# Kernel optimization log

Hardware: AMD Instinct MI355X
Metric: run time of the kernel (lower is better)

Reference implementation:

```python
import jax, jax.numpy as jnp
import numpy as np

ALPHA = 0.5  # trapezoidal_alpha

def rmsnorm(x, w, eps=1e-5):
    return x * jax.lax.rsqrt(jnp.mean(x * x, axis=-1, keepdims=True) + eps) * w

def ssd_scan(x, Bc, Cc, dt, A, alpha):
    # x: (B,L,H,P), Bc/Cc: (B,L,N), dt: (B,L,H), A: (H,)
    da = jnp.exp(dt * A)  # (B,L,H), A < 0 so da in (0,1)
    shift = lambda t: jnp.concatenate([jnp.zeros_like(t[:, :1]), t[:, :-1]], axis=1)
    xp, bp, dtp = shift(x), shift(Bc), shift(dt)
    to_t = lambda t: jnp.moveaxis(t, 1, 0)
    xs = tuple(map(to_t, (x, Bc, Cc, dt, da, xp, bp, dtp)))
    Bb, _, H, P = x.shape
    N = Bc.shape[-1]
    h0 = jnp.zeros((Bb, H, P, N), x.dtype)
    def step(h, inp):
        xt, bt, ct, dtt, dat, xpt, bpt, dtpt = inp
        u = dtt[:, :, None, None] * xt[..., None] * bt[:, None, None, :]      # (B,H,P,N)
        up = dtpt[:, :, None, None] * xpt[..., None] * bpt[:, None, None, :]  # prev input term
        h = dat[:, :, None, None] * (h + alpha * up) + (1.0 - alpha) * u      # trapezoidal update
        y = jnp.einsum('bhpn,bn->bhp', h, ct)
        return h, y
    _, ys = jax.lax.scan(step, h0, xs)
    return jnp.moveaxis(ys, 0, 1)  # (B,L,H,P)

def setup_inputs() -> dict:
    key = jax.random.key(0)
    ks = jax.random.split(key, 10)
    B, NV, NQ = 4, 256, 32
    D, DI, H, N, E, NL = 1024, 2048, 32, 128, 1536, 12
    PROJ = 2 * DI + 2 * N + H  # z | x | B | C | dt
    s = 0.02
    return {
        'visual_tokens': jax.random.normal(ks[0], (B, NV, D), jnp.float32),
        'query_embeds': jax.random.normal(ks[1], (B, NQ, D), jnp.float32),
        'vis_w': jax.random.normal(ks[2], (D, D), jnp.float32) * s,
        'vis_b': jnp.zeros((D,), jnp.float32),
        'qry_w': jax.random.normal(ks[3], (D, D), jnp.float32) * s,
        'qry_b': jnp.zeros((D,), jnp.float32),
        'norm_ws': jnp.ones((NL, D), jnp.float32),
        'in_ws': jax.random.normal(ks[4], (NL, D, PROJ), jnp.float32) * s,
        'dt_biases': jax.random.normal(ks[5], (NL, H), jnp.float32) * 0.5,
        'A_logs': jnp.log(jnp.tile(jnp.arange(1.0, H + 1.0, dtype=jnp.float32)[None], (NL, 1))),
        'D_ssm': jnp.ones((NL, H), jnp.float32),
        'gnorm_ws': jnp.ones((NL, DI), jnp.float32),
        'out_ws': jax.random.normal(ks[6], (NL, DI, D), jnp.float32) * s,
        'norm_f_w': jnp.ones((D,), jnp.float32),
        'head_w': jax.random.normal(ks[7], (D, E), jnp.float32) * s,
        'head_b': jnp.zeros((E,), jnp.float32),
    }

def reference(visual_tokens, query_embeds, vis_w, vis_b, qry_w, qry_b, norm_ws, in_ws,
              dt_biases, A_logs, D_ssm, gnorm_ws, out_ws, norm_f_w, head_w, head_b):
    vis = visual_tokens @ vis_w + vis_b
    qry = query_embeds @ qry_w + qry_b
    hidden = jnp.concatenate([vis, qry], axis=1)  # (B,L,D)
    n_layers = in_ws.shape[0]
    d_inner = gnorm_ws.shape[-1]
    H = A_logs.shape[-1]
    P = d_inner // H
    N = (in_ws.shape[-1] - 2 * d_inner - H) // 2
    for i in range(n_layers):
        res = hidden
        xin = rmsnorm(hidden, norm_ws[i])
        proj = xin @ in_ws[i]  # (B,L,2*DI+2*N+H)
        z = proj[..., :d_inner]
        xss = proj[..., d_inner:2 * d_inner]
        Bc = proj[..., 2 * d_inner:2 * d_inner + N]
        Cc = proj[..., 2 * d_inner + N:2 * d_inner + 2 * N]
        dt = jax.nn.softplus(proj[..., 2 * d_inner + 2 * N:] + dt_biases[i])
        A = -jnp.exp(A_logs[i])
        xr = xss.reshape(xss.shape[0], xss.shape[1], H, P)
        y = ssd_scan(xr, Bc, Cc, dt, A, ALPHA) + D_ssm[i][None, None, :, None] * xr
        y = y.reshape(xss.shape)
        y = rmsnorm(y * jax.nn.silu(z), gnorm_ws[i])  # gated RMSNorm
        hidden = res + y @ out_ws[i]
    hidden = rmsnorm(hidden, norm_f_w)
    pooled = hidden.mean(axis=1)                   # (B,D)
    out = pooled @ head_w + head_b                 # (B,E)
    nrm = jnp.linalg.norm(out, axis=-1, keepdims=True)
    return out / jnp.maximum(nrm, 1e-12)           # F.normalize semantics
```

## Files before the change

kernel.cpp:

```cpp
#include <hip/hip_runtime.h>
#include <cmath>

#define Bb   4
#define Tt   288
#define Dd   1024
#define DIi  2048
#define HH   32
#define PP   64
#define NNs  128
#define PROJ  4384
#define PROJP 4480
#define NLl  12
#define EE   1536

typedef __bf16 bf16x8 __attribute__((ext_vector_type(8)));
typedef float f32x4 __attribute__((ext_vector_type(4)));

__device__ __forceinline__ unsigned short f2bf(float v) {
  __bf16 b = (__bf16)v;
  return __builtin_bit_cast(unsigned short, b);
}
__device__ __forceinline__ float bf2f(unsigned short u) {
  unsigned int x = ((unsigned int)u) << 16;
  return __builtin_bit_cast(float, x);
}
__device__ __forceinline__ void split2(float v, unsigned short& h, unsigned short& l) {
  h = f2bf(v);
  l = f2bf(v - bf2f(h));
}

__device__ __forceinline__ void async16(const void* g, void* l) {
  __builtin_amdgcn_global_load_lds(
      (const __attribute__((address_space(1))) unsigned int*)g,
      (__attribute__((address_space(3))) unsigned int*)l, 16, 0, 0);
}

__device__ inline float block_reduce_sum(float v, float* lds) {
#pragma unroll
  for (int d = 32; d > 0; d >>= 1) v += __shfl_down(v, d, 64);
  int lane = threadIdx.x & 63;
  int w = threadIdx.x >> 6;
  if (lane == 0) lds[w] = v;
  __syncthreads();
  if (threadIdx.x == 0) {
    float s = lds[0];
    int nw = blockDim.x >> 6;
    for (int i = 1; i < nw; i++) s += lds[i];
    lds[0] = s;
  }
  __syncthreads();
  return lds[0];
}

__global__ __launch_bounds__(256) void cvt_act2_k(const float* __restrict__ x,
                                                  unsigned short* __restrict__ oh,
                                                  unsigned short* __restrict__ ol, int n) {
  int idx = (blockIdx.x * 256 + threadIdx.x) * 4;
  if (idx >= n) return;
  float4 v = *(const float4*)&x[idx];
  ushort4 h, l;
  split2(v.x, h.x, l.x); split2(v.y, h.y, l.y);
  split2(v.z, h.z, l.z); split2(v.w, h.w, l.w);
  *(ushort4*)&oh[idx] = h;
  *(ushort4*)&ol[idx] = l;
}

__global__ __launch_bounds__(256) void cvt_tr2_k(const float* __restrict__ W,
                                                 unsigned short* __restrict__ Wth,
                                                 unsigned short* __restrict__ Wtl,
                                                 int K, int N) {
  __shared__ float tile[32][33];
  const int n0 = blockIdx.x * 32, k0 = blockIdx.y * 32;
  const int c = threadIdx.x & 31;
  const int r0 = threadIdx.x >> 5;
#pragma unroll
  for (int j = 0; j < 4; j++) {
    int r = r0 + j * 8;
    int n = n0 + c;
    tile[r][c] = (n < N) ? W[(size_t)(k0 + r) * N + n] : 0.f;
  }
  __syncthreads();
  const int nl = threadIdx.x >> 3;
  const int kl = (threadIdx.x & 7) * 4;
  ushort4 h, l;
  split2(tile[kl + 0][nl], h.x, l.x);
  split2(tile[kl + 1][nl], h.y, l.y);
  split2(tile[kl + 2][nl], h.z, l.z);
  split2(tile[kl + 3][nl], h.w, l.w);
  size_t o = (size_t)(n0 + nl) * K + k0 + kl;
  *(ushort4*)&Wth[o] = h;
  *(ushort4*)&Wtl[o] = l;
}

template<int BM, int BN>
__global__ __launch_bounds__(256) void gemm3_k(
    const unsigned short* __restrict__ Ah, const unsigned short* __restrict__ Al,
    const unsigned short* __restrict__ Wh, const unsigned short* __restrict__ Wl,
    const float* __restrict__ bias, const float* __restrict__ res,
    float* __restrict__ C, int M, int N, int K,
    int rows_per_b, int T_total, int t_off)
{
  constexpr int FM = BM / 32;
  constexpr int FN = BN / 32;
  __shared__ __align__(16) unsigned short Ash[BM * 32];
  __shared__ __align__(16) unsigned short Asl[BM * 32];
  __shared__ __align__(16) unsigned short Bsh[BN * 32];
  __shared__ __align__(16) unsigned short Bsl[BN * 32];
  const int tid = threadIdx.x;
  const int lane = tid & 63;
  const int wm = (tid >> 6) >> 1;
  const int wn = (tid >> 6) & 1;
  const int m0 = blockIdx.y * BM;
  const int n0 = blockIdx.x * BN;
  const int lrow = lane & 15;
  const int lkb = (lane >> 4) * 8;

  f32x4 acc[FM][FN];
#pragma unroll
  for (int i = 0; i < FM; i++)
#pragma unroll
    for (int j = 0; j < FN; j++) acc[i][j] = (f32x4)0.0f;

  for (int k0 = 0; k0 < K; k0 += 32) {
#pragma unroll
    for (int c = 0; c < BM / 64; c++) {
      int o = (c * 256 + tid) * 16;
      int row = o >> 6;
      int colb = o & 63;
      size_t gb = ((size_t)(m0 + row) * K + k0) * 2 + colb;
      async16((const char*)Ah + gb, (char*)Ash + o);
      async16((const char*)Al + gb, (char*)Asl + o);
    }
#pragma unroll
    for (int c = 0; c < BN / 64; c++) {
      int o = (c * 256 + tid) * 16;
      int row = o >> 6;
      int colb = o & 63;
      size_t gb = ((size_t)(n0 + row) * K + k0) * 2 + colb;
      async16((const char*)Wh + gb, (char*)Bsh + o);
      async16((const char*)Wl + gb, (char*)Bsl + o);
    }
    __syncthreads();

    bf16x8 ah[FM], al[FM], bh[FN], bl[FN];
#pragma unroll
    for (int i = 0; i < FM; i++) {
      int off = (wm * (FM * 16) + i * 16 + lrow) * 32 + lkb;
      ah[i] = *(const bf16x8*)&Ash[off];
      al[i] = *(const bf16x8*)&Asl[off];
    }
#pragma unroll
    for (int j = 0; j < FN; j++) {
      int off = (wn * (FN * 16) + j * 16 + lrow) * 32 + lkb;
      bh[j] = *(const bf16x8*)&Bsh[off];
      bl[j] = *(const bf16x8*)&Bsl[off];
    }
#pragma unroll
    for (int i = 0; i < FM; i++)
#pragma unroll
      for (int j = 0; j < FN; j++) {
        acc[i][j] = __builtin_amdgcn_mfma_f32_16x16x32_bf16(ah[i], bh[j], acc[i][j], 0, 0, 0);
        acc[i][j] = __builtin_amdgcn_mfma_f32_16x16x32_bf16(ah[i], bl[j], acc[i][j], 0, 0, 0);
        acc[i][j] = __builtin_amdgcn_mfma_f32_16x16x32_bf16(al[i], bh[j], acc[i][j], 0, 0, 0);
      }
    __syncthreads();
  }

  const int erow = (lane >> 4) * 4;
#pragma unroll
  for (int i = 0; i < FM; i++) {
    int mbase = m0 + wm * (FM * 16) + i * 16 + erow;
#pragma unroll
    for (int j = 0; j < FN; j++) {
      int ncol = n0 + wn * (FN * 16) + j * 16 + lrow;
      float bv = bias ? bias[ncol] : 0.f;
#pragma unroll
      for (int e = 0; e < 4; e++) {
        int m = mbase + e;
        size_t orow;
        if (T_total) {
          int bbv = m / rows_per_b;
          orow = (size_t)bbv * T_total + (m - bbv * rows_per_b) + t_off;
        } else {
          orow = (size_t)m;
        }
        float v = acc[i][j][e] + bv;
        if (res) v += res[orow * N + ncol];
        C[orow * N + ncol] = v;
      }
    }
  }
}

__global__ __launch_bounds__(256) void gemm_k(
    const float* __restrict__ A, const float* __restrict__ W,
    const float* __restrict__ bias, const float* __restrict__ res,
    float* __restrict__ C, int M, int N, int K,
    int rows_per_b, int T_total, int t_off)
{
  __shared__ float As[16][64];
  __shared__ float Ws[16][64];
  const int tid = threadIdx.x;
  const int tx = tid & 15;
  const int ty = tid >> 4;
  const int m0 = blockIdx.y * 64;
  const int n0 = blockIdx.x * 64;
  float acc[4][4] = {};
  const int ar = tid >> 2;
  const int ac = (tid & 3) << 2;
  const int wr = tid >> 4;
  const int wc = (tid & 15) << 2;

  for (int k0 = 0; k0 < K; k0 += 16) {
    float4 av = {0.f, 0.f, 0.f, 0.f};
    int gr = m0 + ar;
    if (gr < M) av = *(const float4*)&A[(size_t)gr * K + k0 + ac];
    As[ac + 0][ar] = av.x; As[ac + 1][ar] = av.y;
    As[ac + 2][ar] = av.z; As[ac + 3][ar] = av.w;

    float4 wv = {0.f, 0.f, 0.f, 0.f};
    int gc = n0 + wc;
    const float* wp = &W[(size_t)(k0 + wr) * N + gc];
    if (gc + 3 < N) {
      wv = *(const float4*)wp;
    } else {
      if (gc + 0 < N) wv.x = wp[0];
      if (gc + 1 < N) wv.y = wp[1];
      if (gc + 2 < N) wv.z = wp[2];
    }
    *(float4*)&Ws[wr][wc] = wv;
    __syncthreads();
#pragma unroll
    for (int kk = 0; kk < 16; kk++) {
      float4 a4 = *(const float4*)&As[kk][ty << 2];
      float4 b4 = *(const float4*)&Ws[kk][tx << 2];
      float a[4] = {a4.x, a4.y, a4.z, a4.w};
      float b[4] = {b4.x, b4.y, b4.z, b4.w};
#pragma unroll
      for (int i = 0; i < 4; i++)
#pragma unroll
        for (int j = 0; j < 4; j++)
          acc[i][j] = fmaf(a[i], b[j], acc[i][j]);
    }
    __syncthreads();
  }
#pragma unroll
  for (int i = 0; i < 4; i++) {
    int gr = m0 + (ty << 2) + i;
    if (gr >= M) continue;
    int bbv = gr / rows_per_b;
    int tt = gr - bbv * rows_per_b;
    size_t orow = (size_t)bbv * T_total + tt + t_off;
#pragma unroll
    for (int j = 0; j < 4; j++) {
      int gc = n0 + (tx << 2) + j;
      if (gc >= N) continue;
      float v = acc[i][j];
      if (bias) v += bias[gc];
      if (res)  v += res[orow * (size_t)N + gc];
      C[orow * (size_t)N + gc] = v;
    }
  }
}

__global__ __launch_bounds__(256) void rmsnorm_k(
    const float* __restrict__ x, const float* __restrict__ w, float* __restrict__ out)
{
  __shared__ float lds[8];
  const int row = blockIdx.x;
  const float* xr = x + (size_t)row * Dd;
  float4 v = *(const float4*)&xr[threadIdx.x << 2];
  float ss = v.x * v.x + v.y * v.y + v.z * v.z + v.w * v.w;
  ss = block_reduce_sum(ss, lds);
  float sc = rsqrtf(ss * (1.f / Dd) + 1e-5f);
  float4 wv = *(const float4*)&w[threadIdx.x << 2];
  float4 o = {v.x * sc * wv.x, v.y * sc * wv.y, v.z * sc * wv.z, v.w * sc * wv.w};
  *(float4*)&out[(size_t)row * Dd + (threadIdx.x << 2)] = o;
}

__global__ __launch_bounds__(256) void rmsnorm2_k(
    const float* __restrict__ x, const float* __restrict__ w,
    unsigned short* __restrict__ oh, unsigned short* __restrict__ ol)
{
  __shared__ float lds[8];
  const int row = blockIdx.x;
  const float* xr = x + (size_t)row * Dd;
  float4 v = *(const float4*)&xr[threadIdx.x << 2];
  float ss = v.x * v.x + v.y * v.y + v.z * v.z + v.w * v.w;
  ss = block_reduce_sum(ss, lds);
  float sc = rsqrtf(ss * (1.f / Dd) + 1e-5f);
  float4 wv = *(const float4*)&w[threadIdx.x << 2];
  ushort4 h, l;
  split2(v.x * sc * wv.x, h.x, l.x);
  split2(v.y * sc * wv.y, h.y, l.y);
  split2(v.z * sc * wv.z, h.z, l.z);
  split2(v.w * sc * wv.w, h.w, l.w);
  size_t o = (size_t)row * Dd + (threadIdx.x << 2);
  *(ushort4*)&oh[o] = h;
  *(ushort4*)&ol[o] = l;
}

__global__ __launch_bounds__(64) void dtcum_k(
    const float* __restrict__ proj, const float* __restrict__ dt_bias,
    const float* __restrict__ A_log,
    float* __restrict__ dtt, double* __restrict__ dcum)
{
  const int h = blockIdx.x & 31;
  const int b = blockIdx.x >> 5;
  const int lane = threadIdx.x;
  const float A = -expf(A_log[h]);
  const float bias = dt_bias[h];
  const int rowo = (b * HH + h) * Tt;
  double base = 0.0;
  for (int c = 0; c < (Tt + 63) / 64; c++) {
    int t = c * 64 + lane;
    float dt = 0.f;
    if (t < Tt) {
      float v = proj[(size_t)(b * Tt + t) * PROJP + 2 * DIi + 2 * NNs + h] + bias;
      dt = (v > 20.f) ? v : log1pf(expf(v));
    }
    double a = (double)(dt * A);
#pragma unroll
    for (int d = 1; d < 64; d <<= 1) {
      double o = __shfl_up(a, d, 64);
      if (lane >= d) a += o;
    }
    double cum = base + a;
    if (t < Tt) { dtt[rowo + t] = dt; dcum[rowo + t] = cum; }
    base = __shfl(cum, 63, 64);
  }
}

__global__ __launch_bounds__(256) void cbgemm_k(const float* __restrict__ proj,
                                                float* __restrict__ St)
{
  const int tI = blockIdx.x, jI = blockIdx.y, b = blockIdx.z;
  if (jI > tI) return;
  __shared__ float Ct[32][130];
  __shared__ float Bt[32][130];
  const int tid = threadIdx.x;
  const int r = tid >> 3;
  const int q = (tid & 7) * 16;
  const float* pb = proj + (size_t)b * Tt * PROJP;
  {
    const float* crow = pb + (size_t)(tI * 32 + r) * PROJP + 2 * DIi + NNs + q;
    const float* brow = pb + (size_t)(jI * 32 + r) * PROJP + 2 * DIi + q;
#pragma unroll
    for (int f = 0; f < 16; f += 4) {
      float4 c4 = *(const float4*)&crow[f];
      float4 b4 = *(const float4*)&brow[f];
      *(float2*)&Ct[r][q + f]     = make_float2(c4.x, c4.y);
      *(float2*)&Ct[r][q + f + 2] = make_float2(c4.z, c4.w);
      *(float2*)&Bt[r][q + f]     = make_float2(b4.x, b4.y);
      *(float2*)&Bt[r][q + f + 2] = make_float2(b4.z, b4.w);
    }
  }
  __syncthreads();
  const int j_r = tid >> 3;
  const int t_c = (tid & 7) * 4;
  float acc[4] = {0.f, 0.f, 0.f, 0.f};
  for (int n = 0; n < NNs; n += 2) {
    float2 b2 = *(const float2*)&Bt[j_r][n];
#pragma unroll
    for (int k = 0; k < 4; k++) {
      float2 c2 = *(const float2*)&Ct[t_c + k][n];
      acc[k] = fmaf(b2.x, c2.x, acc[k]);
      acc[k] = fmaf(b2.y, c2.y, acc[k]);
    }
  }
  float* so = St + ((size_t)b * Tt + jI * 32 + j_r) * Tt + tI * 32 + t_c;
  *(float4*)so = make_float4(acc[0], acc[1], acc[2], acc[3]);
}

__global__ __launch_bounds__(256) void ssd_y_k(
    const float* __restrict__ proj, const float* __restrict__ St,
    const float* __restrict__ dtt, const double* __restrict__ dcum,
    const float* __restrict__ Dssm, float* __restrict__ ybuf)
{
  const int tI = blockIdx.x;
  const int h  = blockIdx.y;
  const int b  = blockIdx.z;
  __shared__ __align__(16) float Xs[32][64];
  __shared__ __align__(16) float Ss[32][36];
  __shared__ double cjs[32];
  const int tid = threadIdx.x;
  const int t_l = tid & 31;
  const int pg  = tid >> 5;
  const int t0  = tI * 32;
  const int rowo = (b * HH + h) * Tt;
  const double ct = dcum[rowo + t0 + t_l];
  const float Ds = Dssm[h];
  const float* pb = proj + (size_t)b * Tt * PROJP;
  float y[8] = {0,0,0,0,0,0,0,0};
  const int sr = tid >> 3;
  const int sq = tid & 7;

  for (int jI = 0; jI <= tI; jI++) {
    const int j0 = jI * 32;
    {
      const float* xr = pb + (size_t)(j0 + sr) * PROJP + DIi + h * PP + sq * 8;
      *(float4*)&Xs[sr][sq * 8]     = *(const float4*)&xr[0];
      *(float4*)&Xs[sr][sq * 8 + 4] = *(const float4*)&xr[4];
    }
    {
      const float* srow = St + ((size_t)b * Tt + j0 + sr) * Tt + t0 + sq * 4;
      float4 s4 = *(const float4*)srow;
      float dj = dtt[rowo + j0 + sr];
      s4.x *= dj; s4.y *= dj; s4.z *= dj; s4.w *= dj;
      *(float4*)&Ss[sr][sq * 4] = s4;
    }
    if (tid < 32) cjs[tid] = dcum[rowo + j0 + tid];
    __syncthreads();

    if (jI < tI) {
#pragma unroll 4
      for (int j = 0; j < 32; j++) {
        float d = (float)(ct - cjs[j]);
        float m = Ss[j][t_l] * expf(fminf(d, 0.f));
        const float* xp = &Xs[j][pg * 8];
        float4 a0 = *(const float4*)&xp[0];
        float4 a1 = *(const float4*)&xp[4];
        y[0] = fmaf(m, a0.x, y[0]); y[1] = fmaf(m, a0.y, y[1]);
        y[2] = fmaf(m, a0.z, y[2]); y[3] = fmaf(m, a0.w, y[3]);
        y[4] = fmaf(m, a1.x, y[4]); y[5] = fmaf(m, a1.y, y[5]);
        y[6] = fmaf(m, a1.z, y[6]); y[7] = fmaf(m, a1.w, y[7]);
      }
    } else {
      for (int j = 0; j < 32; j++) {
        float sv = Ss[j][t_l];
        float d = (float)(ct - cjs[j]);
        float m = sv * expf(fminf(d, 0.f));
        if (j == t_l) m = 0.5f * sv + Ds;
        if (j > t_l)  m = 0.f;
        const float* xp = &Xs[j][pg * 8];
        float4 a0 = *(const float4*)&xp[0];
        float4 a1 = *(const float4*)&xp[4];
        y[0] = fmaf(m, a0.x, y[0]); y[1] = fmaf(m, a0.y, y[1]);
        y[2] = fmaf(m, a0.z, y[2]); y[3] = fmaf(m, a0.w, y[3]);
        y[4] = fmaf(m, a1.x, y[4]); y[5] = fmaf(m, a1.y, y[5]);
        y[6] = fmaf(m, a1.z, y[6]); y[7] = fmaf(m, a1.w, y[7]);
      }
    }
    __syncthreads();
  }
  float* yo = &ybuf[(size_t)(b * Tt + t0 + t_l) * DIi + h * PP + pg * 8];
  *(float4*)&yo[0] = make_float4(y[0], y[1], y[2], y[3]);
  *(float4*)&yo[4] = make_float4(y[4], y[5], y[6], y[7]);
}

__global__ __launch_bounds__(256) void gate_norm2_k(
    const float* __restrict__ ybuf, const float* __restrict__ proj,
    const float* __restrict__ gw,
    unsigned short* __restrict__ yh, unsigned short* __restrict__ yl)
{
  __shared__ float lds[8];
  const int row = blockIdx.x;
  const float* yr = ybuf + (size_t)row * DIi;
  const float* zr = proj + (size_t)row * PROJP;
  const int base = threadIdx.x << 3;
  float4 z0 = *(const float4*)&zr[base];
  float4 z1 = *(const float4*)&zr[base + 4];
  float4 y0 = *(const float4*)&yr[base];
  float4 y1 = *(const float4*)&yr[base + 4];
  float zz[8] = {z0.x, z0.y, z0.z, z0.w, z1.x, z1.y, z1.z, z1.w};
  float yy[8] = {y0.x, y0.y, y0.z, y0.w, y1.x, y1.y, y1.z, y1.w};
  float g[8];
  float ss = 0.f;
#pragma unroll
  for (int e = 0; e < 8; e++) {
    float s = zz[e] / (1.f + expf(-zz[e]));
    float gv = yy[e] * s;
    g[e] = gv;
    ss += gv * gv;
  }
  ss = block_reduce_sum(ss, lds);
  float sc = rsqrtf(ss * (1.f / DIi) + 1e-5f);
  ushort4 h0, l0, h1, l1;
  split2(g[0] * sc * gw[base + 0], h0.x, l0.x);
  split2(g[1] * sc * gw[base + 1], h0.y, l0.y);
  split2(g[2] * sc * gw[base + 2], h0.z, l0.z);
  split2(g[3] * sc * gw[base + 3], h0.w, l0.w);
  split2(g[4] * sc * gw[base + 4], h1.x, l1.x);
  split2(g[5] * sc * gw[base + 5], h1.y, l1.y);
  split2(g[6] * sc * gw[base + 6], h1.z, l1.z);
  split2(g[7] * sc * gw[base + 7], h1.w, l1.w);
  size_t o = (size_t)row * DIi + base;
  *(ushort4*)&yh[o] = h0; *(ushort4*)&yh[o + 4] = h1;
  *(ushort4*)&yl[o] = l0; *(ushort4*)&yl[o + 4] = l1;
}

__global__ void pool_k(const float* __restrict__ xin, float* __restrict__ pooled) {
  int b = blockIdx.x;
  int d = blockIdx.y * 256 + threadIdx.x;
  const float* base = xin + (size_t)b * Tt * Dd + d;
  float s = 0.f;
  for (int t = 0; t < Tt; t++) s += base[(size_t)t * Dd];
  pooled[b * Dd + d] = s * (1.f / Tt);
}

__global__ __launch_bounds__(256) void l2norm_k(float* __restrict__ out) {
  __shared__ float lds[8];
  const int row = blockIdx.x;
  float* r = out + (size_t)row * EE;
  float v[6];
  float ss = 0.f;
#pragma unroll
  for (int e = 0; e < 6; e++) {
    v[e] = r[(e << 8) + threadIdx.x];
    ss += v[e] * v[e];
  }
  ss = block_reduce_sum(ss, lds);
  float sc = 1.f / fmaxf(sqrtf(ss), 1e-12f);
#pragma unroll
  for (int e = 0; e < 6; e++) r[(e << 8) + threadIdx.x] = v[e] * sc;
}

extern "C" void kernel_launch(void* const* d_in, const int* in_sizes, int n_in,
                              void* d_out, int out_size, void* d_ws, size_t ws_size,
                              hipStream_t stream) {
  (void)in_sizes; (void)n_in; (void)out_size; (void)ws_size;
  const float* visual   = (const float*)d_in[0];
  const float* query    = (const float*)d_in[1];
  const float* vis_w    = (const float*)d_in[2];
  const float* vis_b    = (const float*)d_in[3];
  const float* qry_w    = (const float*)d_in[4];
  const float* qry_b    = (const float*)d_in[5];
  const float* norm_ws  = (const float*)d_in[6];
  const float* in_ws    = (const float*)d_in[7];
  const float* dt_biases= (const float*)d_in[8];
  const float* A_logs   = (const float*)d_in[9];
  const float* D_ssm    = (const float*)d_in[10];
  const float* gnorm_ws = (const float*)d_in[11];
  const float* out_ws   = (const float*)d_in[12];
  const float* norm_f_w = (const float*)d_in[13];
  const float* head_w   = (const float*)d_in[14];
  const float* head_b   = (const float*)d_in[15];
  float* out = (float*)d_out;

  char* w = (char*)d_ws;
  float*          hidden = (float*)w;          w += (size_t)1152 * 1024 * 4;
  unsigned short* xh     = (unsigned short*)w; w += (size_t)1152 * 1024 * 2;
  unsigned short* xl     = (unsigned short*)w; w += (size_t)1152 * 1024 * 2;
  float*          proj   = (float*)w;          w += (size_t)1152 * PROJP * 4;
  float*          ybuf   = (float*)w;          w += (size_t)1152 * 2048 * 4;
  unsigned short* yh     = (unsigned short*)w; w += (size_t)1152 * 2048 * 2;
  unsigned short* yl     = (unsigned short*)w; w += (size_t)1152 * 2048 * 2;
  float*          dtt    = (float*)w;          w += (size_t)Bb * HH * Tt * 4;
  double*         dcum   = (double*)w;         w += (size_t)Bb * HH * Tt * 8;
  float*          Stb    = (float*)w;          w += (size_t)Bb * Tt * Tt * 4;
  float*          pooled = (float*)w;          w += (size_t)4096 * 4;
  unsigned short* wth    = (unsigned short*)w; w += (size_t)PROJP * 1024 * 2;
  unsigned short* wtl    = (unsigned short*)w; w += (size_t)PROJP * 1024 * 2;

  dim3 blk(256);

  cvt_act2_k<<<1024, blk, 0, stream>>>(visual, xh, xl, 1024 * 1024);
  cvt_act2_k<<<128, blk, 0, stream>>>(query, xh + (size_t)1024 * 1024,
                                      xl + (size_t)1024 * 1024, 128 * 1024);
  cvt_tr2_k<<<dim3(32, 32), blk, 0, stream>>>(vis_w, wth, wtl, 1024, 1024);
  gemm3_k<64, 64><<<dim3(16, 16), blk, 0, stream>>>(
      xh, xl, wth, wtl, vis_b, nullptr, hidden, 1024, 1024, 1024, 256, Tt, 0);
  cvt_tr2_k<<<dim3(32, 32), blk, 0, stream>>>(qry_w, wth, wtl, 1024, 1024);
  gemm3_k<64, 64><<<dim3(16, 2), blk, 0, stream>>>(
      xh + (size_t)1024 * 1024, xl + (size_t)1024 * 1024, wth, wtl,
      qry_b, nullptr, hidden, 128, 1024, 1024, 32, Tt, 256);

  for (int i = 0; i < NLl; i++) {
    rmsnorm2_k<<<Bb * Tt, blk, 0, stream>>>(hidden, norm_ws + i * Dd, xh, xl);
    cvt_tr2_k<<<dim3(PROJP / 32, 32), blk, 0, stream>>>(
        in_ws + (size_t)i * Dd * PROJ, wth, wtl, Dd, PROJ);
    gemm3_k<128, 128><<<dim3(PROJP / 128, 9), blk, 0, stream>>>(
        xh, xl, wth, wtl, nullptr, nullptr, proj, 1152, PROJP, Dd, 1152, 0, 0);
    dtcum_k<<<Bb * HH, dim3(64), 0, stream>>>(proj, dt_biases + i * HH,
                                              A_logs + i * HH, dtt, dcum);
    cbgemm_k<<<dim3(9, 9, Bb), blk, 0, stream>>>(proj, Stb);
    ssd_y_k<<<dim3(9, HH, Bb), blk, 0, stream>>>(proj, Stb, dtt, dcum,
                                                 D_ssm + i * HH, ybuf);
    gate_norm2_k<<<Bb * Tt, blk, 0, stream>>>(ybuf, proj, gnorm_ws + i * DIi, yh, yl);
    cvt_tr2_k<<<dim3(32, 64), blk, 0, stream>>>(
        out_ws + (size_t)i * DIi * Dd, wth, wtl, DIi, Dd);
    gemm3_k<64, 64><<<dim3(16, 18), blk, 0, stream>>>(
        yh, yl, wth, wtl, nullptr, hidden, hidden, 1152, Dd, DIi, 1152, 0, 0);
  }

  rmsnorm_k<<<Bb * Tt, blk, 0, stream>>>(hidden, norm_f_w, ybuf);
  pool_k<<<dim3(Bb, 4), blk, 0, stream>>>(ybuf, pooled);
  gemm_k<<<dim3(24, 1), blk, 0, stream>>>(pooled, head_w, head_b, nullptr, out,
                                          Bb, EE, Dd, Bb, 0, 0);
  l2norm_k<<<Bb, blk, 0, stream>>>(out);
}
```

Measured before the change: 2.777 ms.

## Use 32x32 MFMA tiles, batch weight conversions upfront, merge activation conversion

Switches the split-bf16 GEMM from 16x16x32 to 32x32x16 MFMA fragments, which changes the per-wave fragment layout and the epilogue indexing. When the workspace is large enough, all layer weights are transposed and split in a few batched launches before the layer loop instead of one conversion per GEMM. The two activation conversion launches are also merged into one. Together these aim to cut launch count and raise MFMA efficiency, at the cost of a much larger workspace and a different accumulator register footprint.

```diff
diff --git a/kernel.cpp b/kernel.cpp
--- a/kernel.cpp
+++ b/kernel.cpp
@@ -15,6 +15,7 @@
 
 typedef __bf16 bf16x8 __attribute__((ext_vector_type(8)));
 typedef float f32x4 __attribute__((ext_vector_type(4)));
+typedef float f32x16 __attribute__((ext_vector_type(16)));
 
 __device__ __forceinline__ unsigned short f2bf(float v) {
   __bf16 b = (__bf16)v;
@@ -52,12 +53,13 @@
   return lds[0];
 }
 
-__global__ __launch_bounds__(256) void cvt_act2_k(const float* __restrict__ x,
-                                                  unsigned short* __restrict__ oh,
-                                                  unsigned short* __restrict__ ol, int n) {
+__global__ __launch_bounds__(256) void cvt_act_k(const float* __restrict__ vis,
+                                                 const float* __restrict__ qry,
+                                                 unsigned short* __restrict__ oh,
+                                                 unsigned short* __restrict__ ol) {
   int idx = (blockIdx.x * 256 + threadIdx.x) * 4;
-  if (idx >= n) return;
-  float4 v = *(const float4*)&x[idx];
+  const float* src = (idx < 1024 * 1024) ? &vis[idx] : &qry[idx - 1024 * 1024];
+  float4 v = *(const float4*)src;
   ushort4 h, l;
   split2(v.x, h.x, l.x); split2(v.y, h.y, l.y);
   split2(v.z, h.z, l.z); split2(v.w, h.w, l.w);
@@ -68,8 +70,12 @@
 __global__ __launch_bounds__(256) void cvt_tr2_k(const float* __restrict__ W,
                                                  unsigned short* __restrict__ Wth,
                                                  unsigned short* __restrict__ Wtl,
-                                                 int K, int N) {
+                                                 int K, int N,
+                                                 size_t wstride, size_t ostride) {
   __shared__ float tile[32][33];
+  W   += (size_t)blockIdx.z * wstride;
+  Wth += (size_t)blockIdx.z * ostride;
+  Wtl += (size_t)blockIdx.z * ostride;
   const int n0 = blockIdx.x * 32, k0 = blockIdx.y * 32;
   const int c = threadIdx.x & 31;
   const int r0 = threadIdx.x >> 5;
@@ -100,8 +106,8 @@
     float* __restrict__ C, int M, int N, int K,
     int rows_per_b, int T_total, int t_off)
 {
-  constexpr int FM = BM / 32;
-  constexpr int FN = BN / 32;
+  constexpr int FM = BM / 64;
+  constexpr int FN = BN / 64;
   __shared__ __align__(16) unsigned short Ash[BM * 32];
   __shared__ __align__(16) unsigned short Asl[BM * 32];
   __shared__ __align__(16) unsigned short Bsh[BN * 32];
@@ -112,14 +118,14 @@
   const int wn = (tid >> 6) & 1;
   const int m0 = blockIdx.y * BM;
   const int n0 = blockIdx.x * BN;
-  const int lrow = lane & 15;
-  const int lkb = (lane >> 4) * 8;
-
-  f32x4 acc[FM][FN];
+  const int lrow = lane & 31;
+  const int lkb = (lane >> 5) * 8;
+
+  f32x16 acc[FM][FN];
 #pragma unroll
   for (int i = 0; i < FM; i++)
 #pragma unroll
-    for (int j = 0; j < FN; j++) acc[i][j] = (f32x4)0.0f;
+    for (int j = 0; j < FN; j++) acc[i][j] = (f32x16)0.0f;
 
   for (int k0 = 0; k0 < K; k0 += 32) {
 #pragma unroll
@@ -142,41 +148,43 @@
     }
     __syncthreads();
 
-    bf16x8 ah[FM], al[FM], bh[FN], bl[FN];
-#pragma unroll
-    for (int i = 0; i < FM; i++) {
-      int off = (wm * (FM * 16) + i * 16 + lrow) * 32 + lkb;
-      ah[i] = *(const bf16x8*)&Ash[off];
-      al[i] = *(const bf16x8*)&Asl[off];
-    }
+#pragma unroll
+    for (int kh = 0; kh < 2; kh++) {
+      bf16x8 ah[FM], al[FM], bh[FN], bl[FN];
+#pragma unroll
+      for (int i = 0; i < FM; i++) {
+        int off = (wm * (BM / 2) + i * 32 + lrow) * 32 + kh * 16 + lkb;
+        ah[i] = *(const bf16x8*)&Ash[off];
+        al[i] = *(const bf16x8*)&Asl[off];
+      }
+#pragma unroll
+      for (int j = 0; j < FN; j++) {
+        int off = (wn * (BN / 2) + j * 32 + lrow) * 32 + kh * 16 + lkb;
+        bh[j] = *(const bf16x8*)&Bsh[off];
+        bl[j] = *(const bf16x8*)&Bsl[off];
+      }
+#pragma unroll
+      for (int i = 0; i < FM; i++)
+#pragma unroll
+        for (int j = 0; j < FN; j++) {
+          acc[i][j] = __builtin_amdgcn_mfma_f32_32x32x16_bf16(ah[i], bh[j], acc[i][j], 0, 0, 0);
+          acc[i][j] = __builtin_amdgcn_mfma_f32_32x32x16_bf16(ah[i], bl[j], acc[i][j], 0, 0, 0);
+          acc[i][j] = __builtin_amdgcn_mfma_f32_32x32x16_bf16(al[i], bh[j], acc[i][j], 0, 0, 0);
+        }
+    }
+    __syncthreads();
+  }
+
+  const int r0 = (lane >> 5) * 4;
+#pragma unroll
+  for (int i = 0; i < FM; i++) {
 #pragma unroll
     for (int j = 0; j < FN; j++) {
-      int off = (wn * (FN * 16) + j * 16 + lrow) * 32 + lkb;
-      bh[j] = *(const bf16x8*)&Bsh[off];
-      bl[j] = *(const bf16x8*)&Bsl[off];
-    }
-#pragma unroll
-    for (int i = 0; i < FM; i++)
-#pragma unroll
-      for (int j = 0; j < FN; j++) {
-        acc[i][j] = __builtin_amdgcn_mfma_f32_16x16x32_bf16(ah[i], bh[j], acc[i][j], 0, 0, 0);
-        acc[i][j] = __builtin_amdgcn_mfma_f32_16x16x32_bf16(ah[i], bl[j], acc[i][j], 0, 0, 0);
-        acc[i][j] = __builtin_amdgcn_mfma_f32_16x16x32_bf16(al[i], bh[j], acc[i][j], 0, 0, 0);
-      }
-    __syncthreads();
-  }
-
-  const int erow = (lane >> 4) * 4;
-#pragma unroll
-  for (int i = 0; i < FM; i++) {
-    int mbase = m0 + wm * (FM * 16) + i * 16 + erow;
-#pragma unroll
-    for (int j = 0; j < FN; j++) {
-      int ncol = n0 + wn * (FN * 16) + j * 16 + lrow;
+      int ncol = n0 + wn * (BN / 2) + j * 32 + lrow;
       float bv = bias ? bias[ncol] : 0.f;
 #pragma unroll
-      for (int e = 0; e < 4; e++) {
-        int m = mbase + e;
+      for (int rg = 0; rg < 16; rg++) {
+        int m = m0 + wm * (BM / 2) + i * 32 + (rg & 3) + 8 * (rg >> 2) + r0;
         size_t orow;
         if (T_total) {
           int bbv = m / rows_per_b;
@@ -184,7 +192,7 @@
         } else {
           orow = (size_t)m;
         }
-        float v = acc[i][j][e] + bv;
+        float v = acc[i][j][rg] + bv;
         if (res) v += res[orow * N + ncol];
         C[orow * N + ncol] = v;
       }
@@ -518,7 +526,7 @@
 extern "C" void kernel_launch(void* const* d_in, const int* in_sizes, int n_in,
                               void* d_out, int out_size, void* d_ws, size_t ws_size,
                               hipStream_t stream) {
-  (void)in_sizes; (void)n_in; (void)out_size; (void)ws_size;
+  (void)in_sizes; (void)n_in; (void)out_size;
   const float* visual   = (const float*)d_in[0];
   const float* query    = (const float*)d_in[1];
   const float* vis_w    = (const float*)d_in[2];
@@ -552,35 +560,72 @@
   unsigned short* wth    = (unsigned short*)w; w += (size_t)PROJP * 1024 * 2;
   unsigned short* wtl    = (unsigned short*)w; w += (size_t)PROJP * 1024 * 2;
 
+  unsigned short* wtin_h  = (unsigned short*)w; w += (size_t)NLl * PROJP * 1024 * 2;
+  unsigned short* wtin_l  = (unsigned short*)w; w += (size_t)NLl * PROJP * 1024 * 2;
+  unsigned short* wtout_h = (unsigned short*)w; w += (size_t)NLl * 1024 * 2048 * 2;
+  unsigned short* wtout_l = (unsigned short*)w; w += (size_t)NLl * 1024 * 2048 * 2;
+  unsigned short* wtv_h   = (unsigned short*)w; w += (size_t)1024 * 1024 * 2;
+  unsigned short* wtv_l   = (unsigned short*)w; w += (size_t)1024 * 1024 * 2;
+  unsigned short* wtq_h   = (unsigned short*)w; w += (size_t)1024 * 1024 * 2;
+  unsigned short* wtq_l   = (unsigned short*)w; w += (size_t)1024 * 1024 * 2;
+  const bool batched = ((size_t)(w - (char*)d_ws)) <= ws_size;
+
   dim3 blk(256);
 
-  cvt_act2_k<<<1024, blk, 0, stream>>>(visual, xh, xl, 1024 * 1024);
-  cvt_act2_k<<<128, blk, 0, stream>>>(query, xh + (size_t)1024 * 1024,
-                                      xl + (size_t)1024 * 1024, 128 * 1024);
-  cvt_tr2_k<<<dim3(32, 32), blk, 0, stream>>>(vis_w, wth, wtl, 1024, 1024);
-  gemm3_k<64, 64><<<dim3(16, 16), blk, 0, stream>>>(
-      xh, xl, wth, wtl, vis_b, nullptr, hidden, 1024, 1024, 1024, 256, Tt, 0);
-  cvt_tr2_k<<<dim3(32, 32), blk, 0, stream>>>(qry_w, wth, wtl, 1024, 1024);
-  gemm3_k<64, 64><<<dim3(16, 2), blk, 0, stream>>>(
-      xh + (size_t)1024 * 1024, xl + (size_t)1024 * 1024, wth, wtl,
-      qry_b, nullptr, hidden, 128, 1024, 1024, 32, Tt, 256);
+  cvt_act_k<<<1152, blk, 0, stream>>>(visual, query, xh, xl);
+
+  if (batched) {
+    cvt_tr2_k<<<dim3(32, 32, 1), blk, 0, stream>>>(vis_w, wtv_h, wtv_l, 1024, 1024, 0, 0);
+    cvt_tr2_k<<<dim3(32, 32, 1), blk, 0, stream>>>(qry_w, wtq_h, wtq_l, 1024, 1024, 0, 0);
+    cvt_tr2_k<<<dim3(PROJP / 32, 32, NLl), blk, 0, stream>>>(
+        in_ws, wtin_h, wtin_l, Dd, PROJ, (size_t)Dd * PROJ, (size_t)PROJP * 1024);
+    cvt_tr2_k<<<dim3(32, 64, NLl), blk, 0, stream>>>(
+        out_ws, wtout_h, wtout_l, DIi, Dd, (size_t)DIi * Dd, (size_t)1024 * 2048);
+    gemm3_k<64, 64><<<dim3(16, 16), blk, 0, stream>>>(
+        xh, xl, wtv_h, wtv_l, vis_b, nullptr, hidden, 1024, 1024, 1024, 256, Tt, 0);
+    gemm3_k<64, 64><<<dim3(16, 2), blk, 0, stream>>>(
+        xh + (size_t)1024 * 1024, xl + (size_t)1024 * 1024, wtq_h, wtq_l,
+        qry_b, nullptr, hidden, 128, 1024, 1024, 32, Tt, 256);
+  } else {
+    cvt_tr2_k<<<dim3(32, 32, 1), blk, 0, stream>>>(vis_w, wth, wtl, 1024, 1024, 0, 0);
+    gemm3_k<64, 64><<<dim3(16, 16), blk, 0, stream>>>(
+        xh, xl, wth, wtl, vis_b, nullptr, hidden, 1024, 1024, 1024, 256, Tt, 0);
+    cvt_tr2_k<<<dim3(32, 32, 1), blk, 0, stream>>>(qry_w, wth, wtl, 1024, 1024, 0, 0);
+    gemm3_k<64, 64><<<dim3(16, 2), blk, 0, stream>>>(
+        xh + (size_t)1024 * 1024, xl + (size_t)1024 * 1024, wth, wtl,
+        qry_b, nullptr, hidden, 128, 1024, 1024, 32, Tt, 256);
+  }
 
   for (int i = 0; i < NLl; i++) {
     rmsnorm2_k<<<Bb * Tt, blk, 0, stream>>>(hidden, norm_ws + i * Dd, xh, xl);
-    cvt_tr2_k<<<dim3(PROJP / 32, 32), blk, 0, stream>>>(
-        in_ws + (size_t)i * Dd * PROJ, wth, wtl, Dd, PROJ);
+    const unsigned short *bih, *bil;
+    if (batched) {
+      bih = wtin_h + (size_t)i * PROJP * 1024;
+      bil = wtin_l + (size_t)i * PROJP * 1024;
+    } else {
+      cvt_tr2_k<<<dim3(PROJP / 32, 32, 1), blk, 0, stream>>>(
+          in_ws + (size_t)i * Dd * PROJ, wth, wtl, Dd, PROJ, 0, 0);
+      bih = wth; bil = wtl;
+    }
     gemm3_k<128, 128><<<dim3(PROJP / 128, 9), blk, 0, stream>>>(
-        xh, xl, wth, wtl, nullptr, nullptr, proj, 1152, PROJP, Dd, 1152, 0, 0);
+        xh, xl, bih, bil, nullptr, nullptr, proj, 1152, PROJP, Dd, 1152, 0, 0);
     dtcum_k<<<Bb * HH, dim3(64), 0, stream>>>(proj, dt_biases + i * HH,
                                               A_logs + i * HH, dtt, dcum);
     cbgemm_k<<<dim3(9, 9, Bb), blk, 0, stream>>>(proj, Stb);
     ssd_y_k<<<dim3(9, HH, Bb), blk, 0, stream>>>(proj, Stb, dtt, dcum,
                                                  D_ssm + i * HH, ybuf);
     gate_norm2_k<<<Bb * Tt, blk, 0, stream>>>(ybuf, proj, gnorm_ws + i * DIi, yh, yl);
-    cvt_tr2_k<<<dim3(32, 64), blk, 0, stream>>>(
-        out_ws + (size_t)i * DIi * Dd, wth, wtl, DIi, Dd);
+    const unsigned short *boh, *bol;
+    if (batched) {
+      boh = wtout_h + (size_t)i * 1024 * 2048;
+      bol = wtout_l + (size_t)i * 1024 * 2048;
+    } else {
+      cvt_tr2_k<<<dim3(32, 64, 1), blk, 0, stream>>>(
+          out_ws + (size_t)i * DIi * Dd, wth, wtl, DIi, Dd, 0, 0);
+      boh = wth; bol = wtl;
+    }
     gemm3_k<64, 64><<<dim3(16, 18), blk, 0, stream>>>(
-        yh, yl, wth, wtl, nullptr, hidden, hidden, 1152, Dd, DIi, 1152, 0, 0);
+        yh, yl, boh, bol, nullptr, hidden, hidden, 1152, Dd, DIi, 1152, 0, 0);
   }
 
   rmsnorm_k<<<Bb * Tt, blk, 0, stream>>>(hidden, norm_f_w, ybuf);
```

Measured after the change: 2.935 ms. 1.06x slower.
